# Kernel tuning notes

Measured on AMD Instinct MI355X. Metric: run time of the kernel, lower is better.

## Reference

```python
import jax, jax.numpy as jnp
import numpy as np

VOCAB, D, H = 32000, 1024, 16
DH = D // H
DFF = 4 * D
EPS = 1e-5


def layer_norm(x, g, b):
    mu = jnp.mean(x, axis=-1, keepdims=True)
    var = jnp.var(x, axis=-1, keepdims=True)
    return (x - mu) * jax.lax.rsqrt(var + EPS) * g + b


def pos_enc(seq_len, d_model):
    # faithful to the torch double-loop: angle = pos / 10000**(2*i/d) for even index i
    pos = jnp.arange(seq_len, dtype=jnp.float32)[:, None]          # [S,1]
    i_even = jnp.arange(0, d_model, 2, dtype=jnp.float32)[None, :]  # [1,D/2]
    angle = pos / jnp.power(10000.0, 2.0 * i_even / d_model)        # [S,D/2]
    pe = jnp.zeros((seq_len, d_model), dtype=jnp.float32)
    pe = pe.at[:, 0::2].set(jnp.sin(angle))
    pe = pe.at[:, 1::2].set(jnp.cos(angle))
    return pe


def setup_inputs() -> dict:
    key = jax.random.key(0)
    ks = jax.random.split(key, 16)
    s = 0.02
    return {
        "tokens": jax.random.randint(ks[0], (4, 2048), 0, VOCAB),
        "emb": jax.random.normal(ks[1], (VOCAB, D), jnp.float32) * s,
        "in_proj_w": jax.random.normal(ks[2], (3 * D, D), jnp.float32) * s,
        "in_proj_b": jnp.zeros((3 * D,), jnp.float32),
        "out_proj_w": jax.random.normal(ks[3], (D, D), jnp.float32) * s,
        "out_proj_b": jnp.zeros((D,), jnp.float32),
        "w1": jax.random.normal(ks[4], (DFF, D), jnp.float32) * s,
        "b1": jnp.zeros((DFF,), jnp.float32),
        "w2": jax.random.normal(ks[5], (D, DFF), jnp.float32) * s,
        "b2": jnp.zeros((D,), jnp.float32),
        "g1": jnp.ones((D,), jnp.float32),
        "beta1": jnp.zeros((D,), jnp.float32),
        "g2": jnp.ones((D,), jnp.float32),
        "beta2": jnp.zeros((D,), jnp.float32),
    }


def reference(tokens, emb, in_proj_w, in_proj_b, out_proj_w, out_proj_b,
              w1, b1, w2, b2, g1, beta1, g2, beta2):
    B, S = tokens.shape
    x = emb[tokens] + pos_enc(S, D)[None, :, :]                 # [B,S,D]
    # multi-head self-attention (eval mode, no dropout)
    qkv = x @ in_proj_w.T + in_proj_b                           # [B,S,3D]
    q, k, v = jnp.split(qkv, 3, axis=-1)
    q = q.reshape(B, S, H, DH)
    k = k.reshape(B, S, H, DH)
    v = v.reshape(B, S, H, DH)
    scores = jnp.einsum("bqhd,bkhd->bhqk", q, k) / jnp.sqrt(jnp.float32(DH))
    attn = jax.nn.softmax(scores, axis=-1)
    ctx = jnp.einsum("bhqk,bkhd->bqhd", attn, v).reshape(B, S, D)
    attn_out = ctx @ out_proj_w.T + out_proj_b
    h = layer_norm(x + attn_out, g1, beta1)
    ff = jax.nn.relu(h @ w1.T + b1) @ w2.T + b2
    return layer_norm(h + ff, g2, beta2)
```

## Files before the change

### kernel.cpp

```cpp
#include <hip/hip_runtime.h>
#include <math.h>

#define DMODEL 1024
#define NH 16
#define DHEAD 64
#define DFF 4096
#define BATCH 4
#define SEQ 2048
#define MROWS (BATCH * SEQ)
#define LNEPS 1e-5f
#define NT (SEQ / 64)

typedef __attribute__((ext_vector_type(8))) short bf16x8;
typedef __attribute__((ext_vector_type(4))) float f32x4;
typedef __attribute__((ext_vector_type(16))) float f32x16;
typedef __attribute__((ext_vector_type(4))) unsigned int u32x4;

__device__ inline unsigned short f2bf(float f) {
  unsigned int u = __float_as_uint(f);
  unsigned int r = (u + 0x7fffu + ((u >> 16) & 1u)) >> 16;
  return (unsigned short)r;
}

__device__ inline void gload16(const unsigned short* g, char* l) {
  __builtin_amdgcn_global_load_lds(
      (const __attribute__((address_space(1))) unsigned int*)g,
      (__attribute__((address_space(3))) unsigned int*)l, 16, 0, 0);
}

__device__ inline float fexp2(float x) {
  float r;
  asm("v_exp_f32 %0, %1" : "=v"(r) : "v"(x));
  return r;
}
__device__ inline unsigned int cvtpk(float lo, float hi) {
  unsigned int r;
  asm("v_cvt_pk_bf16_f32 %0, %1, %2" : "=v"(r) : "v"(lo), "v"(hi));
  return r;
}
__device__ inline void plswap(unsigned int& a, unsigned int& b) {
  asm("v_permlane32_swap_b32 %0, %1" : "+v"(a), "+v"(b));
}

__global__ __launch_bounds__(256)
void embed_kernel(const int* __restrict__ tokens, const float* __restrict__ emb,
                  float* __restrict__ X, unsigned short* __restrict__ Xb) {
  const int HALF = DMODEL / 2;
  int idx = blockIdx.x * 256 + threadIdx.x;
  if (idx >= MROWS * HALF) return;
  int row = idx / HALF;
  int j = idx - row * HALF;
  int s = row & (SEQ - 1);
  int tok = tokens[row];
  float2 e = ((const float2*)(emb + (size_t)tok * DMODEL))[j];
  float denom = powf(10000.0f, (2.0f * (float)(2 * j)) / (float)DMODEL);
  float ang = (float)s / denom;
  float sn, cs;
  sincosf(ang, &sn, &cs);
  float2 o;
  o.x = e.x + sn;
  o.y = e.y + cs;
  ((float2*)(X + (size_t)row * DMODEL))[j] = o;
  ushort2 ob;
  ob.x = f2bf(o.x); ob.y = f2bf(o.y);
  ((ushort2*)(Xb + (size_t)row * DMODEL))[j] = ob;
}

__global__ __launch_bounds__(256)
void cvt4_kernel(const float* __restrict__ a, const float* __restrict__ b,
                 const float* __restrict__ c, const float* __restrict__ d,
                 unsigned short* __restrict__ oa, unsigned short* __restrict__ ob,
                 unsigned short* __restrict__ oc, unsigned short* __restrict__ od) {
  int i = blockIdx.x * 256 + threadIdx.x;
  const float* src; unsigned short* dst; int off;
  if (i < 786432)       { src = a; dst = oa; off = 0; }
  else if (i < 1048576) { src = b; dst = ob; off = 786432; }
  else if (i < 2097152) { src = c; dst = oc; off = 1048576; }
  else                  { src = d; dst = od; off = 2097152; }
  int j = i - off;
  float4 v = ((const float4*)src)[j];
  ushort4 o;
  o.x = f2bf(v.x); o.y = f2bf(v.y); o.z = f2bf(v.z); o.w = f2bf(v.w);
  ((ushort4*)dst)[j] = o;
}

__device__ inline void sthalf8(const unsigned short* G, int grow0, int K, int kt,
                               char* smem_, int isB, int half, int t) {
  char* dst = smem_ + ((kt & 1) * 65536) + isB * 32768 + half * 16384;
#pragma unroll
  for (int i = 0; i < 2; ++i) {
    int g = i * 512 + t;
    int r = g >> 3, sl = g & 7;
    int c = sl ^ (r & 7);
    gload16(G + (size_t)(grow0 + half * 128 + r) * K + kt * 64 + c * 8, dst + g * 16);
  }
}

#define VM4_ asm volatile("s_waitcnt vmcnt(4)" ::: "memory")
#define VM0_ asm volatile("s_waitcnt vmcnt(0)" ::: "memory")

#define PHASE8(bufofs, MG, NP, LA, LB, STAGE_STMT, WAIT_STMT)                   \
  {                                                                             \
    if (LA) {                                                                   \
      _Pragma("unroll") for (int m = 0; m < 4; ++m) {                           \
        int arow = wm * 128 + (MG) * 64 + m * 16 + fr;                          \
        _Pragma("unroll") for (int ks = 0; ks < 2; ++ks)                        \
          af[m][ks] = *(const bf16x8*)(smem + (bufofs) + arow * 128 +           \
                        (((ks * 4 + fq) ^ (arow & 7)) * 16));                   \
      }                                                                         \
    }                                                                           \
    if (LB) {                                                                   \
      _Pragma("unroll") for (int nn = 0; nn < 2; ++nn) {                        \
        int n = (NP) * 2 + nn;                                                  \
        int brow = wn * 64 + n * 16 + fr;                                       \
        _Pragma("unroll") for (int ks = 0; ks < 2; ++ks)                        \
          bf[(NP) * 2 + nn][ks] = *(const bf16x8*)(smem + (bufofs) + 32768 +    \
                        brow * 128 + (((ks * 4 + fq) ^ (brow & 7)) * 16));      \
      }                                                                         \
    }                                                                           \
    STAGE_STMT;                                                                 \
    __builtin_amdgcn_sched_barrier(0);                                          \
    __builtin_amdgcn_s_barrier();                                               \
    asm volatile("s_waitcnt lgkmcnt(0)" ::: "memory");                          \
    __builtin_amdgcn_sched_barrier(0);                                          \
    __builtin_amdgcn_s_setprio(1);                                              \
    _Pragma("unroll") for (int m = 0; m < 4; ++m)                               \
      _Pragma("unroll") for (int nn = 0; nn < 2; ++nn)                          \
        _Pragma("unroll") for (int ks = 0; ks < 2; ++ks)                        \
          acc[(MG) * 4 + m][(NP) * 2 + nn] =                                    \
              __builtin_amdgcn_mfma_f32_16x16x32_bf16(                          \
                  af[m][ks], bf[(NP) * 2 + nn][ks],                             \
                  acc[(MG) * 4 + m][(NP) * 2 + nn], 0, 0, 0);                   \
    __builtin_amdgcn_s_setprio(0);                                              \
    WAIT_STMT;                                                                  \
    __builtin_amdgcn_sched_barrier(0);                                          \
    __builtin_amdgcn_s_barrier();                                               \
    __builtin_amdgcn_sched_barrier(0);                                          \
  }

__global__ __launch_bounds__(512, 2)
void gemm8p(const unsigned short* __restrict__ A, const unsigned short* __restrict__ B,
            const float* __restrict__ bias, const float* __restrict__ resid,
            float* __restrict__ Cf, unsigned short* __restrict__ Cb,
            int M, int N, int K, int relu) {
  extern __shared__ char smem[];

  const int t = threadIdx.x;
  const int lane = t & 63;
  const int wv = t >> 6;
  const int wm = wv >> 2;
  const int wn = wv & 3;
  const int fr = lane & 15;
  const int fq = lane >> 4;

  const int nwg = gridDim.x;
  const int orig = blockIdx.x;
  const int q8 = nwg >> 3;
  const int wgid = (orig & 7) * q8 + (orig >> 3);
  const int stid = wgid >> 2, within = wgid & 3;
  const int sm = within & 1, sn = within >> 1;
  const int Msup = M >> 9;
  const int stm = stid % Msup, stn = stid / Msup;
  const int m0 = (stm * 2 + sm) * 256;
  const int n0 = (stn * 2 + sn) * 256;

  f32x4 acc[8][4];
#pragma unroll
  for (int m = 0; m < 8; ++m)
#pragma unroll
    for (int n = 0; n < 4; ++n) acc[m][n] = (f32x4){0.f, 0.f, 0.f, 0.f};

  const int nk = K / 64;
  const int nj = nk / 2;

  sthalf8(A, m0, K, 0, smem, 0, 0, t);
  sthalf8(A, m0, K, 0, smem, 0, 1, t);
  sthalf8(B, n0, K, 0, smem, 1, 0, t);
  sthalf8(B, n0, K, 0, smem, 1, 1, t);
  sthalf8(B, n0, K, 1, smem, 1, 0, t);
  sthalf8(B, n0, K, 1, smem, 1, 1, t);
  VM4_;
  __builtin_amdgcn_sched_barrier(0);
  __builtin_amdgcn_s_barrier();
  __builtin_amdgcn_sched_barrier(0);

  bf16x8 af[4][2];
  bf16x8 bf[4][2];

  for (int j = 0; j < nj; ++j) {
    const bool st = (j + 1 < nj);
    PHASE8(0, 0, 0, 1, 1, sthalf8(A, m0, K, 2 * j + 1, smem, 0, 0, t), );
    PHASE8(0, 0, 1, 0, 1, sthalf8(A, m0, K, 2 * j + 1, smem, 0, 1, t), );
    PHASE8(0, 1, 1, 1, 0,
           if (st) sthalf8(B, n0, K, 2 * j + 2, smem, 1, 0, t), );
    PHASE8(0, 1, 0, 0, 0,
           if (st) sthalf8(B, n0, K, 2 * j + 2, smem, 1, 1, t),
           { if (st) { VM4_; } else { VM0_; } });
    PHASE8(65536, 0, 0, 1, 1,
           if (st) sthalf8(A, m0, K, 2 * j + 2, smem, 0, 0, t), );
    PHASE8(65536, 0, 1, 0, 1,
           if (st) sthalf8(A, m0, K, 2 * j + 2, smem, 0, 1, t), );
    PHASE8(65536, 1, 1, 1, 0,
           if (st) sthalf8(B, n0, K, 2 * j + 3, smem, 1, 0, t), );
    PHASE8(65536, 1, 0, 0, 0,
           if (st) sthalf8(B, n0, K, 2 * j + 3, smem, 1, 1, t),
           { if (st) { VM4_; } });
  }

  float* slab = (float*)(smem + wv * 4352);
#pragma unroll
  for (int m = 0; m < 8; ++m) {
#pragma unroll
    for (int n = 0; n < 4; ++n)
#pragma unroll
      for (int j = 0; j < 4; ++j)
        slab[(fq * 4 + j) * 68 + n * 16 + fr] = acc[m][n][j];
    int rg0 = m0 + wm * 128 + m * 16;
#pragma unroll
    for (int it = 0; it < 4; ++it) {
      int u = it * 64 + lane;
      int row = u >> 4, seg = u & 15;
      float4 v = *(const float4*)&slab[row * 68 + seg * 4];
      int col = n0 + wn * 64 + seg * 4;
      float4 b4 = *(const float4*)&bias[col];
      v.x += b4.x; v.y += b4.y; v.z += b4.z; v.w += b4.w;
      if (relu) {
        v.x = fmaxf(v.x, 0.f); v.y = fmaxf(v.y, 0.f);
        v.z = fmaxf(v.z, 0.f); v.w = fmaxf(v.w, 0.f);
      }
      size_t idx = (size_t)(rg0 + row) * N + col;
      if (resid) {
        float4 r4 = *(const float4*)&resid[idx];
        v.x += r4.x; v.y += r4.y; v.z += r4.z; v.w += r4.w;
      }
      if (Cf) {
        *(float4*)&Cf[idx] = v;
      } else {
        ushort4 ob;
        ob.x = f2bf(v.x); ob.y = f2bf(v.y); ob.z = f2bf(v.z); ob.w = f2bf(v.w);
        *(ushort4*)&Cb[idx] = ob;
      }
    }
  }
}

#define AOFF(buf) ((buf) * 49152)
#define BOFF(buf) ((buf) * 49152 + 32768)

__device__ inline void stageA(const unsigned short* Ag, char* smem_, int buf,
                              int m0, int K, int kt, int wv, int lane) {
  int rl = lane >> 3, c = (lane & 7) ^ rl;
#pragma unroll
  for (int i = 0; i < 4; ++i) {
    int r0 = (wv * 4 + i) * 8;
    gload16(Ag + (size_t)(m0 + r0 + rl) * K + kt * 64 + c * 8,
            smem_ + AOFF(buf) + r0 * 128 + lane * 16);
  }
}
__device__ inline void stageB2(const unsigned short* Bg, char* smem_, int buf,
                               int n0, int K, int kt, int wv, int lane) {
  int rl = lane >> 3, c = (lane & 7) ^ rl;
#pragma unroll
  for (int i = 0; i < 2; ++i) {
    int r0 = (wv * 2 + i) * 8;
    gload16(Bg + (size_t)(n0 + r0 + rl) * K + kt * 64 + c * 8,
            smem_ + BOFF(buf) + r0 * 128 + lane * 16);
  }
}

#define VM6 asm volatile("s_waitcnt vmcnt(6)" ::: "memory")
#define VM0 asm volatile("s_waitcnt vmcnt(0)" ::: "memory")

#define DO_PHASE(buf, mb, LOADB, STAGE_STMT, WAIT_STMT)                         \
  {                                                                             \
    bf16x8 af[2][2];                                                            \
    _Pragma("unroll") for (int mm = 0; mm < 2; ++mm) {                          \
      int arow = wm * 64 + ((mb) + mm) * 16 + fr;                               \
      _Pragma("unroll") for (int ks = 0; ks < 2; ++ks) {                        \
        int slot = (ks * 4 + fq) ^ (arow & 7);                                  \
        af[mm][ks] = *(const bf16x8*)(smem + AOFF(buf) + arow * 128 + slot * 16); \
      }                                                                         \
    }                                                                           \
    if (LOADB) {                                                                \
      _Pragma("unroll") for (int n = 0; n < 4; ++n) {                           \
        int brow = wn * 64 + n * 16 + fr;                                       \
        _Pragma("unroll") for (int ks = 0; ks < 2; ++ks) {                      \
          int slot = (ks * 4 + fq) ^ (brow & 7);                                \
          bfr[n][ks] = *(const bf16x8*)(smem + BOFF(buf) + brow * 128 + slot * 16); \
        }                                                                       \
      }                                                                         \
    }                                                                           \
    STAGE_STMT;                                                                 \
    __builtin_amdgcn_sched_barrier(0);                                          \
    __builtin_amdgcn_s_barrier();                                               \
    __builtin_amdgcn_sched_barrier(0);                                          \
    __builtin_amdgcn_s_setprio(1);                                              \
    _Pragma("unroll") for (int mm = 0; mm < 2; ++mm)                            \
      _Pragma("unroll") for (int n = 0; n < 4; ++n)                             \
        _Pragma("unroll") for (int ks = 0; ks < 2; ++ks)                        \
          acc[(mb) + mm][n] = __builtin_amdgcn_mfma_f32_16x16x32_bf16(          \
              af[mm][ks], bfr[n][ks], acc[(mb) + mm][n], 0, 0, 0);              \
    __builtin_amdgcn_s_setprio(0);                                              \
    WAIT_STMT;                                                                  \
    __builtin_amdgcn_sched_barrier(0);                                          \
    __builtin_amdgcn_s_barrier();                                               \
    __builtin_amdgcn_sched_barrier(0);                                          \
  }

__global__ __launch_bounds__(512, 2)
void gemm8(const unsigned short* __restrict__ A, const unsigned short* __restrict__ B,
           const float* __restrict__ bias, const float* __restrict__ resid,
           float* __restrict__ Cf, unsigned short* __restrict__ Cb,
           int M, int N, int K, int relu) {
  extern __shared__ char smem[];

  const int t = threadIdx.x;
  const int lane = t & 63;
  const int wv = t >> 6;
  const int wm = wv >> 1;
  const int wn = wv & 1;
  const int fr = lane & 15;
  const int fq = lane >> 4;

  const int nwg = gridDim.x;
  const int orig = blockIdx.x;
  const int q8 = nwg >> 3;
  const int wgid = (orig & 7) * q8 + (orig >> 3);
  const int stid = wgid >> 4, within = wgid & 15;
  const int sm = within & 3, sn = within >> 2;
  const int Msup = M >> 10;
  const int stm = stid % Msup, stn = stid / Msup;
  const int m0 = (stm * 4 + sm) * 256;
  const int n0 = (stn * 4 + sn) * 128;

  f32x4 acc[4][4];
#pragma unroll
  for (int m = 0; m < 4; ++m)
#pragma unroll
    for (int n = 0; n < 4; ++n) acc[m][n] = (f32x4){0.f, 0.f, 0.f, 0.f};

  const int nk = K / 64;
  const int nj = nk / 2;

  stageB2(B, smem, 0, n0, K, 0, wv, lane);
  stageA (A, smem, 0, m0, K, 0, wv, lane);
  stageB2(B, smem, 1, n0, K, 1, wv, lane);
  stageA (A, smem, 1, m0, K, 1, wv, lane);
  VM6;
  __builtin_amdgcn_sched_barrier(0);
  __builtin_amdgcn_s_barrier();
  __builtin_amdgcn_sched_barrier(0);

  for (int j = 0; j < nj - 1; ++j) {
    const int k0 = 2 * j, k1 = 2 * j + 1;
    const int s0k = k0 + 2, s1k = k1 + 2;
    const int b0 = k0 % 3, b1 = k1 % 3;
    const int sb0 = s0k % 3, sb1 = s1k % 3;
    bf16x8 bfr[4][2];
    DO_PHASE(b0, 0, true,  stageB2(B, smem, sb0, n0, K, s0k, wv, lane), );
    DO_PHASE(b0, 2, false, stageA (A, smem, sb0, m0, K, s0k, wv, lane), VM6);
    DO_PHASE(b1, 0, true,  stageB2(B, smem, sb1, n0, K, s1k, wv, lane), );
    DO_PHASE(b1, 2, false, stageA (A, smem, sb1, m0, K, s1k, wv, lane), VM6);
  }
  {
    const int b0 = (nk - 2) % 3, b1 = (nk - 1) % 3;
    bf16x8 bfr[4][2];
    DO_PHASE(b0, 0, true,  , );
    DO_PHASE(b0, 2, false, , VM0);
    DO_PHASE(b1, 0, true,  , );
    DO_PHASE(b1, 2, false, , );
  }

  float* slab = (float*)(smem + wv * 4352);
#pragma unroll
  for (int m = 0; m < 4; ++m) {
#pragma unroll
    for (int n = 0; n < 4; ++n)
#pragma unroll
      for (int j = 0; j < 4; ++j)
        slab[(fq * 4 + j) * 68 + n * 16 + fr] = acc[m][n][j];
    int rg0 = m0 + wm * 64 + m * 16;
#pragma unroll
    for (int it = 0; it < 4; ++it) {
      int u = it * 64 + lane;
      int row = u >> 4, seg = u & 15;
      float4 v = *(const float4*)&slab[row * 68 + seg * 4];
      int col = n0 + wn * 64 + seg * 4;
      float4 b4 = *(const float4*)&bias[col];
      v.x += b4.x; v.y += b4.y; v.z += b4.z; v.w += b4.w;
      if (relu) {
        v.x = fmaxf(v.x, 0.f); v.y = fmaxf(v.y, 0.f);
        v.z = fmaxf(v.z, 0.f); v.w = fmaxf(v.w, 0.f);
      }
      size_t idx = (size_t)(rg0 + row) * N + col;
      if (resid) {
        float4 r4 = *(const float4*)&resid[idx];
        v.x += r4.x; v.y += r4.y; v.z += r4.z; v.w += r4.w;
      }
      if (Cf) {
        *(float4*)&Cf[idx] = v;
      } else {
        ushort4 ob;
        ob.x = f2bf(v.x); ob.y = f2bf(v.y); ob.z = f2bf(v.z); ob.w = f2bf(v.w);
        *(ushort4*)&Cb[idx] = ob;
      }
    }
  }
}

__global__ __launch_bounds__(256)
void vtrans_kernel(const unsigned short* __restrict__ qkvb, unsigned short* __restrict__ vtb) {
  __shared__ __align__(16) unsigned short tile[64][64];
  const int st = blockIdx.x;
  const int bh = blockIdx.y;
  const int b = bh >> 4, h = bh & 15;
  const int t = threadIdx.x;
#pragma unroll
  for (int p = 0; p < 2; ++p) {
    int item = p * 256 + t;
    int r = item >> 3, c8 = item & 7;
    const unsigned short* src =
        qkvb + (size_t)(b * SEQ + st * 64 + r) * (3 * DMODEL) + 2048 + h * 64 + c8 * 8;
    *(uint4*)&tile[r][(c8 ^ (r & 7)) * 8] = *(const uint4*)src;
  }
  __syncthreads();
#pragma unroll
  for (int p = 0; p < 2; ++p) {
    int item = p * 256 + t;
    int d = item & 63, s8 = item >> 6;
    unsigned short v[8];
#pragma unroll
    for (int e = 0; e < 8; ++e) {
      int s = s8 * 8 + e;
      v[e] = tile[s][(((d >> 3) ^ (s & 7)) * 8) + (d & 7)];
    }
    uint4 u;
    u.x = (unsigned int)v[0] | ((unsigned int)v[1] << 16);
    u.y = (unsigned int)v[2] | ((unsigned int)v[3] << 16);
    u.z = (unsigned int)v[4] | ((unsigned int)v[5] << 16);
    u.w = (unsigned int)v[6] | ((unsigned int)v[7] << 16);
    *(uint4*)(vtb + ((size_t)bh * 64 + d) * SEQ + st * 64 + s8 * 8) = u;
  }
}

__global__ __launch_bounds__(512, 4)
void attn_kernel(const unsigned short* __restrict__ qkv, const unsigned short* __restrict__ vtb,
                 unsigned short* __restrict__ ctxb) {
  __shared__ __align__(16) unsigned short Ks[2][64][64];
  __shared__ __align__(16) unsigned short Vts[2][64][64];
  __shared__ __align__(16) unsigned short Slab[8][32][64];

  const int t = threadIdx.x;
  const int lane = t & 63;
  const int wq = t >> 6;
  const int l31 = lane & 31;
  const int hi1 = lane >> 5;
  const int bid = blockIdx.x;
  const int bh = bid & 63;
  const int qt = bid >> 6;
  const int b = bh >> 4, h = bh & 15;
  const int q0 = qt * 256;

  const size_t RS = 3 * DMODEL;
  const unsigned short* qb = qkv + (size_t)b * SEQ * RS + h * DHEAD;
  const unsigned short* kb = qb + DMODEL;

  bf16x8 qf[4];
  {
    const unsigned short* qrow = qb + (size_t)(q0 + wq * 32 + l31) * RS;
#pragma unroll
    for (int s = 0; s < 4; ++s)
      qf[s] = *(const bf16x8*)(qrow + s * 16 + hi1 * 8);
  }

  const unsigned short* kgl =
      kb + (size_t)(wq * 8 + (lane >> 3)) * RS + ((lane & 7) ^ (lane >> 3)) * 8;
  const unsigned short* vgl =
      vtb + ((size_t)bh * 64 + wq * 8 + (lane >> 3)) * SEQ + ((lane & 7) ^ (lane >> 3)) * 8;

  f32x16 oacc[2] = {};
  float lacc = 0.f;

  gload16(kgl, (char*)&Ks[0][wq * 8][0]);
  gload16(vgl, (char*)&Vts[0][wq * 8][0]);
  __syncthreads();

  const float C = 0.18033688011112042f;

  for (int kt = 0; kt < NT; ++kt) {
    const int cur = kt & 1;
    if (kt + 1 < NT) {
      gload16(kgl + (size_t)(kt + 1) * 64 * RS, (char*)&Ks[cur ^ 1][wq * 8][0]);
      gload16(vgl + (size_t)(kt + 1) * 64, (char*)&Vts[cur ^ 1][wq * 8][0]);
    }

    f32x16 sacc[2] = {};
    __builtin_amdgcn_s_setprio(1);
#pragma unroll
    for (int s = 0; s < 4; ++s) {
#pragma unroll
      for (int kvt = 0; kvt < 2; ++kvt) {
        int row = kvt * 32 + l31;
        bf16x8 kf = *(const bf16x8*)&Ks[cur][row][(((2 * s + hi1) ^ (row & 7)) * 8)];
        sacc[kvt] = __builtin_amdgcn_mfma_f32_32x32x16_bf16(kf, qf[s], sacc[kvt], 0, 0, 0);
      }
    }
    __builtin_amdgcn_s_setprio(0);

#pragma unroll
    for (int kvt = 0; kvt < 2; ++kvt) {
      float p[16];
#pragma unroll
      for (int r = 0; r < 16; ++r) p[r] = fexp2(sacc[kvt][r] * C);
      float ps = 0.f;
#pragma unroll
      for (int r = 0; r < 16; ++r) ps += p[r];
      lacc += ps;
#pragma unroll
      for (int half = 0; half < 2; ++half) {
        const int lo = half * 8;
        unsigned int x0 = cvtpk(p[lo + 0], p[lo + 1]);
        unsigned int x1 = cvtpk(p[lo + 2], p[lo + 3]);
        unsigned int y0 = cvtpk(p[lo + 4], p[lo + 5]);
        unsigned int y1 = cvtpk(p[lo + 6], p[lo + 7]);
        plswap(x0, y0);
        plswap(x1, y1);
        bf16x8 pa = __builtin_bit_cast(bf16x8, (u32x4){x0, x1, y0, y1});
        const int s2 = kvt * 2 + half;
        __builtin_amdgcn_s_setprio(1);
#pragma unroll
        for (int dt = 0; dt < 2; ++dt) {
          int vrow = dt * 32 + l31;
          bf16x8 vf = *(const bf16x8*)&Vts[cur][vrow][(((2 * s2 + hi1) ^ (vrow & 7)) * 8)];
          oacc[dt] = __builtin_amdgcn_mfma_f32_32x32x16_bf16(pa, vf, oacc[dt], 0, 0, 0);
        }
        __builtin_amdgcn_s_setprio(0);
      }
    }
    __syncthreads();
  }

  lacc += __shfl_xor(lacc, 32);
  float inv = 1.0f / lacc;

  float iv[16];
#pragma unroll
  for (int r = 0; r < 16; ++r)
    iv[r] = __shfl(inv, (r & 3) + 8 * (r >> 2) + 4 * hi1);

#pragma unroll
  for (int dt = 0; dt < 2; ++dt) {
    const int chunk = dt * 4 + (l31 >> 3);
    const int e7 = l31 & 7;
#pragma unroll
    for (int r = 0; r < 16; ++r) {
      int qp = (r & 3) + 8 * (r >> 2) + 4 * hi1;
      Slab[wq][qp][((chunk ^ (qp & 7)) * 8) + e7] = f2bf(oacc[dt][r] * iv[r]);
    }
  }
#pragma unroll
  for (int it = 0; it < 4; ++it) {
    int u = it * 64 + lane;
    int row = u >> 3, s = u & 7;
    uint4 v = *(const uint4*)&Slab[wq][row][((s ^ (row & 7)) * 8)];
    *(uint4*)(ctxb + (size_t)(b * SEQ + q0 + wq * 32 + row) * DMODEL + h * DHEAD + s * 8) = v;
  }
}

__global__ __launch_bounds__(256)
void ln_kernel(const float* __restrict__ Z, const float* __restrict__ g,
               const float* __restrict__ bta, float* __restrict__ Y,
               unsigned short* __restrict__ Yb) {
  const int row = blockIdx.x;
  const float4* z4 = (const float4*)(Z + (size_t)row * DMODEL);
  float4 v = z4[threadIdx.x];
  float s = v.x + v.y + v.z + v.w;
  float ss = fmaf(v.x, v.x, fmaf(v.y, v.y, fmaf(v.z, v.z, v.w * v.w)));
#pragma unroll
  for (int o = 32; o >= 1; o >>= 1) {
    s += __shfl_xor(s, o);
    ss += __shfl_xor(ss, o);
  }
  __shared__ float red[8];
  int w = threadIdx.x >> 6;
  if ((threadIdx.x & 63) == 0) { red[w] = s; red[4 + w] = ss; }
  __syncthreads();
  s = red[0] + red[1] + red[2] + red[3];
  ss = red[4] + red[5] + red[6] + red[7];
  float mu = s * (1.0f / DMODEL);
  float var = ss * (1.0f / DMODEL) - mu * mu;
  float rs = rsqrtf(var + LNEPS);
  float4 gg = ((const float4*)g)[threadIdx.x];
  float4 bb = ((const float4*)bta)[threadIdx.x];
  float4 o;
  o.x = (v.x - mu) * rs * gg.x + bb.x;
  o.y = (v.y - mu) * rs * gg.y + bb.y;
  o.z = (v.z - mu) * rs * gg.z + bb.z;
  o.w = (v.w - mu) * rs * gg.w + bb.w;
  ((float4*)(Y + (size_t)row * DMODEL))[threadIdx.x] = o;
  if (Yb) {
    ushort4 ob;
    ob.x = f2bf(o.x); ob.y = f2bf(o.y); ob.z = f2bf(o.z); ob.w = f2bf(o.w);
    ((ushort4*)(Yb + (size_t)row * DMODEL))[threadIdx.x] = ob;
  }
}

extern "C" void kernel_launch(void* const* d_in, const int* in_sizes, int n_in,
                              void* d_out, int out_size, void* d_ws, size_t ws_size,
                              hipStream_t stream) {
  const int* tokens       = (const int*)d_in[0];
  const float* emb        = (const float*)d_in[1];
  const float* in_proj_w  = (const float*)d_in[2];
  const float* in_proj_b  = (const float*)d_in[3];
  const float* out_proj_w = (const float*)d_in[4];
  const float* out_proj_b = (const float*)d_in[5];
  const float* w1         = (const float*)d_in[6];
  const float* b1         = (const float*)d_in[7];
  const float* w2         = (const float*)d_in[8];
  const float* b2         = (const float*)d_in[9];
  const float* g1         = (const float*)d_in[10];
  const float* beta1      = (const float*)d_in[11];
  const float* g2         = (const float*)d_in[12];
  const float* beta2      = (const float*)d_in[13];
  float* out = (float*)d_out;

  char* ws = (char*)d_ws;
  const size_t MB = 1ull << 20;
  unsigned short* inwb  = (unsigned short*)(ws + 0 * MB);
  unsigned short* outwb = (unsigned short*)(ws + 6 * MB);
  unsigned short* w1b   = (unsigned short*)(ws + 8 * MB);
  unsigned short* w2b   = (unsigned short*)(ws + 16 * MB);
  float* x              = (float*)(ws + 24 * MB);
  unsigned short* xb    = (unsigned short*)(ws + 56 * MB);
  unsigned short* qkvb  = (unsigned short*)(ws + 72 * MB);
  unsigned short* vtb   = (unsigned short*)(ws + 120 * MB);
  unsigned short* ctxb  = (unsigned short*)(ws + 56 * MB);
  float* h              = (float*)(ws + 72 * MB);
  unsigned short* hb    = (unsigned short*)(ws + 104 * MB);
  unsigned short* ffbb  = (unsigned short*)(ws + 120 * MB);
  float* y2             = (float*)(ws + 24 * MB);

  const size_t GLDS8 = 147456;
  const size_t GLDSP = 131072;

  embed_kernel<<<(MROWS * (DMODEL / 2) + 255) / 256, 256, 0, stream>>>(tokens, emb, x, xb);
  cvt4_kernel<<<12288, 256, 0, stream>>>(in_proj_w, out_proj_w, w1, w2,
                                         inwb, outwb, w1b, w2b);
  gemm8p<<<(MROWS / 256) * (3 * DMODEL / 256), 512, GLDSP, stream>>>(
      xb, inwb, in_proj_b, nullptr, nullptr, qkvb, MROWS, 3 * DMODEL, DMODEL, 0);
  vtrans_kernel<<<dim3(SEQ / 64, BATCH * NH), 256, 0, stream>>>(qkvb, vtb);
  attn_kernel<<<(SEQ / 256) * (BATCH * NH), 512, 0, stream>>>(qkvb, vtb, ctxb);
  gemm8<<<(MROWS / 256) * (DMODEL / 128), 512, GLDS8, stream>>>(
      ctxb, outwb, out_proj_b, x, h, nullptr, MROWS, DMODEL, DMODEL, 0);
  ln_kernel<<<MROWS, 256, 0, stream>>>(h, g1, beta1, h, hb);
  gemm8p<<<(MROWS / 256) * (DFF / 256), 512, GLDSP, stream>>>(
      hb, w1b, b1, nullptr, nullptr, ffbb, MROWS, DFF, DMODEL, 1);
  gemm8<<<(MROWS / 256) * (DMODEL / 128), 512, GLDS8, stream>>>(
      ffbb, w2b, b2, h, y2, nullptr, MROWS, DMODEL, DFF, 0);
  ln_kernel<<<MROWS, 256, 0, stream>>>(y2, g2, beta2, out, nullptr);
}
```

Measured before the change: 400.9 us.

## Process two query subtiles per warp in attention to reuse K/V fragments

Each attention workgroup now covers 512 query rows instead of 256, with every warp holding two 32-row query fragments and two sets of accumulators. Each K and V fragment read from LDS feeds two MFMAs, halving the K/V global loads and LDS reads per query. The grid shrinks to 256 blocks. Register pressure doubles, so launch bounds drop to 2 blocks per CU, which reduces occupancy and the ability to hide latency.

Result: no change. 407.7 us (+1.7%).

```diff
diff --git a/kernel.cpp b/kernel.cpp
--- a/kernel.cpp
+++ b/kernel.cpp
@@ -443,7 +443,7 @@
   }
 }
 
-__global__ __launch_bounds__(512, 4)
+__global__ __launch_bounds__(512, 2)
 void attn_kernel(const unsigned short* __restrict__ qkv, const unsigned short* __restrict__ vtb,
                  unsigned short* __restrict__ ctxb) {
   __shared__ __align__(16) unsigned short Ks[2][64][64];
@@ -459,18 +459,21 @@
   const int bh = bid & 63;
   const int qt = bid >> 6;
   const int b = bh >> 4, h = bh & 15;
-  const int q0 = qt * 256;
+  const int q0 = qt * 512;
 
   const size_t RS = 3 * DMODEL;
   const unsigned short* qb = qkv + (size_t)b * SEQ * RS + h * DHEAD;
   const unsigned short* kb = qb + DMODEL;
 
-  bf16x8 qf[4];
+  bf16x8 qf0[4], qf1[4];
   {
-    const unsigned short* qrow = qb + (size_t)(q0 + wq * 32 + l31) * RS;
-#pragma unroll
-    for (int s = 0; s < 4; ++s)
-      qf[s] = *(const bf16x8*)(qrow + s * 16 + hi1 * 8);
+    const unsigned short* qr0 = qb + (size_t)(q0 + wq * 64 + l31) * RS;
+    const unsigned short* qr1 = qr0 + 32 * RS;
+#pragma unroll
+    for (int s = 0; s < 4; ++s) {
+      qf0[s] = *(const bf16x8*)(qr0 + s * 16 + hi1 * 8);
+      qf1[s] = *(const bf16x8*)(qr1 + s * 16 + hi1 * 8);
+    }
   }
 
   const unsigned short* kgl =
@@ -478,8 +481,9 @@
   const unsigned short* vgl =
       vtb + ((size_t)bh * 64 + wq * 8 + (lane >> 3)) * SEQ + ((lane & 7) ^ (lane >> 3)) * 8;
 
-  f32x16 oacc[2] = {};
-  float lacc = 0.f;
+  f32x16 oacc0[2] = {};
+  f32x16 oacc1[2] = {};
+  float lacc0 = 0.f, lacc1 = 0.f;
 
   gload16(kgl, (char*)&Ks[0][wq * 8][0]);
   gload16(vgl, (char*)&Vts[0][wq * 8][0]);
@@ -494,7 +498,8 @@
       gload16(vgl + (size_t)(kt + 1) * 64, (char*)&Vts[cur ^ 1][wq * 8][0]);
     }
 
-    f32x16 sacc[2] = {};
+    f32x16 sacc0[2] = {};
+    f32x16 sacc1[2] = {};
     __builtin_amdgcn_s_setprio(1);
 #pragma unroll
     for (int s = 0; s < 4; ++s) {
@@ -502,68 +507,98 @@
       for (int kvt = 0; kvt < 2; ++kvt) {
         int row = kvt * 32 + l31;
         bf16x8 kf = *(const bf16x8*)&Ks[cur][row][(((2 * s + hi1) ^ (row & 7)) * 8)];
-        sacc[kvt] = __builtin_amdgcn_mfma_f32_32x32x16_bf16(kf, qf[s], sacc[kvt], 0, 0, 0);
+        sacc0[kvt] = __builtin_amdgcn_mfma_f32_32x32x16_bf16(kf, qf0[s], sacc0[kvt], 0, 0, 0);
+        sacc1[kvt] = __builtin_amdgcn_mfma_f32_32x32x16_bf16(kf, qf1[s], sacc1[kvt], 0, 0, 0);
       }
     }
     __builtin_amdgcn_s_setprio(0);
 
+    bf16x8 pa0[4], pa1[4];
 #pragma unroll
     for (int kvt = 0; kvt < 2; ++kvt) {
-      float p[16];
-#pragma unroll
-      for (int r = 0; r < 16; ++r) p[r] = fexp2(sacc[kvt][r] * C);
-      float ps = 0.f;
-#pragma unroll
-      for (int r = 0; r < 16; ++r) ps += p[r];
-      lacc += ps;
+      float p0[16], p1[16];
+#pragma unroll
+      for (int r = 0; r < 16; ++r) p0[r] = fexp2(sacc0[kvt][r] * C);
+#pragma unroll
+      for (int r = 0; r < 16; ++r) p1[r] = fexp2(sacc1[kvt][r] * C);
+      float ps0 = 0.f, ps1 = 0.f;
+#pragma unroll
+      for (int r = 0; r < 16; ++r) { ps0 += p0[r]; ps1 += p1[r]; }
+      lacc0 += ps0;
+      lacc1 += ps1;
 #pragma unroll
       for (int half = 0; half < 2; ++half) {
         const int lo = half * 8;
-        unsigned int x0 = cvtpk(p[lo + 0], p[lo + 1]);
-        unsigned int x1 = cvtpk(p[lo + 2], p[lo + 3]);
-        unsigned int y0 = cvtpk(p[lo + 4], p[lo + 5]);
-        unsigned int y1 = cvtpk(p[lo + 6], p[lo + 7]);
-        plswap(x0, y0);
-        plswap(x1, y1);
-        bf16x8 pa = __builtin_bit_cast(bf16x8, (u32x4){x0, x1, y0, y1});
-        const int s2 = kvt * 2 + half;
-        __builtin_amdgcn_s_setprio(1);
-#pragma unroll
-        for (int dt = 0; dt < 2; ++dt) {
-          int vrow = dt * 32 + l31;
-          bf16x8 vf = *(const bf16x8*)&Vts[cur][vrow][(((2 * s2 + hi1) ^ (vrow & 7)) * 8)];
-          oacc[dt] = __builtin_amdgcn_mfma_f32_32x32x16_bf16(pa, vf, oacc[dt], 0, 0, 0);
+        {
+          unsigned int x0 = cvtpk(p0[lo + 0], p0[lo + 1]);
+          unsigned int x1 = cvtpk(p0[lo + 2], p0[lo + 3]);
+          unsigned int y0 = cvtpk(p0[lo + 4], p0[lo + 5]);
+          unsigned int y1 = cvtpk(p0[lo + 6], p0[lo + 7]);
+          plswap(x0, y0);
+          plswap(x1, y1);
+          pa0[kvt * 2 + half] = __builtin_bit_cast(bf16x8, (u32x4){x0, x1, y0, y1});
         }
-        __builtin_amdgcn_s_setprio(0);
-      }
-    }
+        {
+          unsigned int x0 = cvtpk(p1[lo + 0], p1[lo + 1]);
+          unsigned int x1 = cvtpk(p1[lo + 2], p1[lo + 3]);
+          unsigned int y0 = cvtpk(p1[lo + 4], p1[lo + 5]);
+          unsigned int y1 = cvtpk(p1[lo + 6], p1[lo + 7]);
+          plswap(x0, y0);
+          plswap(x1, y1);
+          pa1[kvt * 2 + half] = __builtin_bit_cast(bf16x8, (u32x4){x0, x1, y0, y1});
+        }
+      }
+    }
+
+    __builtin_amdgcn_s_setprio(1);
+#pragma unroll
+    for (int s2 = 0; s2 < 4; ++s2) {
+#pragma unroll
+      for (int dt = 0; dt < 2; ++dt) {
+        int vrow = dt * 32 + l31;
+        bf16x8 vf = *(const bf16x8*)&Vts[cur][vrow][(((2 * s2 + hi1) ^ (vrow & 7)) * 8)];
+        oacc0[dt] = __builtin_amdgcn_mfma_f32_32x32x16_bf16(pa0[s2], vf, oacc0[dt], 0, 0, 0);
+        oacc1[dt] = __builtin_amdgcn_mfma_f32_32x32x16_bf16(pa1[s2], vf, oacc1[dt], 0, 0, 0);
+      }
+    }
+    __builtin_amdgcn_s_setprio(0);
     __syncthreads();
   }
 
-  lacc += __shfl_xor(lacc, 32);
-  float inv = 1.0f / lacc;
-
-  float iv[16];
-#pragma unroll
-  for (int r = 0; r < 16; ++r)
-    iv[r] = __shfl(inv, (r & 3) + 8 * (r >> 2) + 4 * hi1);
-
-#pragma unroll
-  for (int dt = 0; dt < 2; ++dt) {
-    const int chunk = dt * 4 + (l31 >> 3);
-    const int e7 = l31 & 7;
-#pragma unroll
-    for (int r = 0; r < 16; ++r) {
-      int qp = (r & 3) + 8 * (r >> 2) + 4 * hi1;
-      Slab[wq][qp][((chunk ^ (qp & 7)) * 8) + e7] = f2bf(oacc[dt][r] * iv[r]);
-    }
-  }
-#pragma unroll
-  for (int it = 0; it < 4; ++it) {
-    int u = it * 64 + lane;
-    int row = u >> 3, s = u & 7;
-    uint4 v = *(const uint4*)&Slab[wq][row][((s ^ (row & 7)) * 8)];
-    *(uint4*)(ctxb + (size_t)(b * SEQ + q0 + wq * 32 + row) * DMODEL + h * DHEAD + s * 8) = v;
+  lacc0 += __shfl_xor(lacc0, 32);
+  lacc1 += __shfl_xor(lacc1, 32);
+  float inv0 = 1.0f / lacc0;
+  float inv1 = 1.0f / lacc1;
+
+  float iv0[16], iv1[16];
+#pragma unroll
+  for (int r = 0; r < 16; ++r) {
+    int qp = (r & 3) + 8 * (r >> 2) + 4 * hi1;
+    iv0[r] = __shfl(inv0, qp);
+    iv1[r] = __shfl(inv1, qp);
+  }
+
+#pragma unroll
+  for (int qi = 0; qi < 2; ++qi) {
+#pragma unroll
+    for (int dt = 0; dt < 2; ++dt) {
+      const int chunk = dt * 4 + (l31 >> 3);
+      const int e7 = l31 & 7;
+#pragma unroll
+      for (int r = 0; r < 16; ++r) {
+        int qp = (r & 3) + 8 * (r >> 2) + 4 * hi1;
+        float val = (qi == 0) ? oacc0[dt][r] * iv0[r] : oacc1[dt][r] * iv1[r];
+        Slab[wq][qp][((chunk ^ (qp & 7)) * 8) + e7] = f2bf(val);
+      }
+    }
+#pragma unroll
+    for (int it = 0; it < 4; ++it) {
+      int u = it * 64 + lane;
+      int row = u >> 3, s = u & 7;
+      uint4 v = *(const uint4*)&Slab[wq][row][((s ^ (row & 7)) * 8)];
+      *(uint4*)(ctxb + (size_t)(b * SEQ + q0 + wq * 64 + qi * 32 + row) * DMODEL +
+                h * DHEAD + s * 8) = v;
+    }
   }
 }
 
@@ -649,7 +684,7 @@
   gemm8p<<<(MROWS / 256) * (3 * DMODEL / 256), 512, GLDSP, stream>>>(
       xb, inwb, in_proj_b, nullptr, nullptr, qkvb, MROWS, 3 * DMODEL, DMODEL, 0);
   vtrans_kernel<<<dim3(SEQ / 64, BATCH * NH), 256, 0, stream>>>(qkvb, vtb);
-  attn_kernel<<<(SEQ / 256) * (BATCH * NH), 512, 0, stream>>>(qkvb, vtb, ctxb);
+  attn_kernel<<<(SEQ / 512) * (BATCH * NH), 512, 0, stream>>>(qkvb, vtb, ctxb);
   gemm8<<<(MROWS / 256) * (DMODEL / 128), 512, GLDS8, stream>>>(
       ctxb, outwb, out_proj_b, x, h, nullptr, MROWS, DMODEL, DMODEL, 0);
   ln_kernel<<<MROWS, 256, 0, stream>>>(h, g1, beta1, h, hb);
```

## Rewrite N=1024 GEMM with 8-phase double-buffered pipeline and smaller LDS

Applied to the files above, without the earlier changes.

Replaces the triple-buffered 4-phase gemm8 used for the out-projection and FFN2 GEMMs with a gemm8p128 kernel. It mirrors the 8-phase ping-pong schedule of gemm8p, using two LDS buffers (96KB instead of 144KB) and staging A and B in half-tile chunks interleaved across eight MFMA phases. It also changes the workgroup swizzle from 4x4 to 2x2 supertiles and adds an explicit lgkmcnt wait after each barrier. The aim is finer overlap of global loads with MFMA and lower LDS use, at the cost of less prefetch depth and more barriers.

Measured after the change: 401.1 us. No clear change (+0.0%).

```diff
diff --git a/kernel.cpp b/kernel.cpp
--- a/kernel.cpp
+++ b/kernel.cpp
@@ -97,6 +97,7 @@
 }
 
 #define VM4_ asm volatile("s_waitcnt vmcnt(4)" ::: "memory")
+#define VM2_ asm volatile("s_waitcnt vmcnt(2)" ::: "memory")
 #define VM0_ asm volatile("s_waitcnt vmcnt(0)" ::: "memory")
 
 #define PHASE8(bufofs, MG, NP, LA, LB, STAGE_STMT, WAIT_STMT)                   \
@@ -244,62 +245,61 @@
   }
 }
 
-#define AOFF(buf) ((buf) * 49152)
-#define BOFF(buf) ((buf) * 49152 + 32768)
-
-__device__ inline void stageA(const unsigned short* Ag, char* smem_, int buf,
-                              int m0, int K, int kt, int wv, int lane) {
-  int rl = lane >> 3, c = (lane & 7) ^ rl;
-#pragma unroll
-  for (int i = 0; i < 4; ++i) {
-    int r0 = (wv * 4 + i) * 8;
-    gload16(Ag + (size_t)(m0 + r0 + rl) * K + kt * 64 + c * 8,
-            smem_ + AOFF(buf) + r0 * 128 + lane * 16);
-  }
-}
-__device__ inline void stageB2(const unsigned short* Bg, char* smem_, int buf,
-                               int n0, int K, int kt, int wv, int lane) {
-  int rl = lane >> 3, c = (lane & 7) ^ rl;
+__device__ inline void stA128(const unsigned short* G, int m0, int K, int kt,
+                              int half, char* smem_, int t) {
+  char* dst = smem_ + ((kt & 1) * 49152) + half * 16384;
 #pragma unroll
   for (int i = 0; i < 2; ++i) {
-    int r0 = (wv * 2 + i) * 8;
-    gload16(Bg + (size_t)(n0 + r0 + rl) * K + kt * 64 + c * 8,
-            smem_ + BOFF(buf) + r0 * 128 + lane * 16);
-  }
-}
-
-#define VM6 asm volatile("s_waitcnt vmcnt(6)" ::: "memory")
-#define VM0 asm volatile("s_waitcnt vmcnt(0)" ::: "memory")
-
-#define DO_PHASE(buf, mb, LOADB, STAGE_STMT, WAIT_STMT)                         \
+    int g = i * 512 + t;
+    int r = g >> 3, sl = g & 7;
+    int c = sl ^ (r & 7);
+    gload16(G + (size_t)(m0 + half * 128 + r) * K + kt * 64 + c * 8, dst + g * 16);
+  }
+}
+__device__ inline void stB128(const unsigned short* G, int n0, int K, int kt,
+                              char* smem_, int t) {
+  char* dst = smem_ + ((kt & 1) * 49152) + 32768;
+#pragma unroll
+  for (int i = 0; i < 2; ++i) {
+    int g = i * 512 + t;
+    int r = g >> 3, sl = g & 7;
+    int c = sl ^ (r & 7);
+    gload16(G + (size_t)(n0 + r) * K + kt * 64 + c * 8, dst + g * 16);
+  }
+}
+
+#define PH128(bufofs, MG, NP, LA, LB, STAGE_STMT, WAIT_STMT)                    \
   {                                                                             \
-    bf16x8 af[2][2];                                                            \
-    _Pragma("unroll") for (int mm = 0; mm < 2; ++mm) {                          \
-      int arow = wm * 64 + ((mb) + mm) * 16 + fr;                               \
-      _Pragma("unroll") for (int ks = 0; ks < 2; ++ks) {                        \
-        int slot = (ks * 4 + fq) ^ (arow & 7);                                  \
-        af[mm][ks] = *(const bf16x8*)(smem + AOFF(buf) + arow * 128 + slot * 16); \
+    if (LA) {                                                                   \
+      _Pragma("unroll") for (int mm = 0; mm < 2; ++mm) {                        \
+        int arow = wm * 64 + ((MG) * 2 + mm) * 16 + fr;                         \
+        _Pragma("unroll") for (int ks = 0; ks < 2; ++ks)                        \
+          af[mm][ks] = *(const bf16x8*)(smem + (bufofs) + arow * 128 +          \
+                        (((ks * 4 + fq) ^ (arow & 7)) * 16));                   \
       }                                                                         \
     }                                                                           \
-    if (LOADB) {                                                                \
-      _Pragma("unroll") for (int n = 0; n < 4; ++n) {                           \
+    if (LB) {                                                                   \
+      _Pragma("unroll") for (int nn = 0; nn < 2; ++nn) {                        \
+        int n = (NP) * 2 + nn;                                                  \
         int brow = wn * 64 + n * 16 + fr;                                       \
-        _Pragma("unroll") for (int ks = 0; ks < 2; ++ks) {                      \
-          int slot = (ks * 4 + fq) ^ (brow & 7);                                \
-          bfr[n][ks] = *(const bf16x8*)(smem + BOFF(buf) + brow * 128 + slot * 16); \
-        }                                                                       \
+        _Pragma("unroll") for (int ks = 0; ks < 2; ++ks)                        \
+          bf[(NP) * 2 + nn][ks] = *(const bf16x8*)(smem + (bufofs) + 32768 +    \
+                        brow * 128 + (((ks * 4 + fq) ^ (brow & 7)) * 16));      \
       }                                                                         \
     }                                                                           \
     STAGE_STMT;                                                                 \
     __builtin_amdgcn_sched_barrier(0);                                          \
     __builtin_amdgcn_s_barrier();                                               \
+    asm volatile("s_waitcnt lgkmcnt(0)" ::: "memory");                          \
     __builtin_amdgcn_sched_barrier(0);                                          \
     __builtin_amdgcn_s_setprio(1);                                              \
     _Pragma("unroll") for (int mm = 0; mm < 2; ++mm)                            \
-      _Pragma("unroll") for (int n = 0; n < 4; ++n)                             \
+      _Pragma("unroll") for (int nn = 0; nn < 2; ++nn)                          \
         _Pragma("unroll") for (int ks = 0; ks < 2; ++ks)                        \
-          acc[(mb) + mm][n] = __builtin_amdgcn_mfma_f32_16x16x32_bf16(          \
-              af[mm][ks], bfr[n][ks], acc[(mb) + mm][n], 0, 0, 0);              \
+          acc[(MG) * 2 + mm][(NP) * 2 + nn] =                                   \
+              __builtin_amdgcn_mfma_f32_16x16x32_bf16(                          \
+                  af[mm][ks], bf[(NP) * 2 + nn][ks],                            \
+                  acc[(MG) * 2 + mm][(NP) * 2 + nn], 0, 0, 0);                  \
     __builtin_amdgcn_s_setprio(0);                                              \
     WAIT_STMT;                                                                  \
     __builtin_amdgcn_sched_barrier(0);                                          \
@@ -308,10 +308,10 @@
   }
 
 __global__ __launch_bounds__(512, 2)
-void gemm8(const unsigned short* __restrict__ A, const unsigned short* __restrict__ B,
-           const float* __restrict__ bias, const float* __restrict__ resid,
-           float* __restrict__ Cf, unsigned short* __restrict__ Cb,
-           int M, int N, int K, int relu) {
+void gemm8p128(const unsigned short* __restrict__ A, const unsigned short* __restrict__ B,
+               const float* __restrict__ bias, const float* __restrict__ resid,
+               float* __restrict__ Cf, unsigned short* __restrict__ Cb,
+               int M, int N, int K, int relu) {
   extern __shared__ char smem[];
 
   const int t = threadIdx.x;
@@ -326,12 +326,12 @@
   const int orig = blockIdx.x;
   const int q8 = nwg >> 3;
   const int wgid = (orig & 7) * q8 + (orig >> 3);
-  const int stid = wgid >> 4, within = wgid & 15;
-  const int sm = within & 3, sn = within >> 2;
-  const int Msup = M >> 10;
+  const int stid = wgid >> 2, within = wgid & 3;
+  const int sm = within & 1, sn = within >> 1;
+  const int Msup = M >> 9;
   const int stm = stid % Msup, stn = stid / Msup;
-  const int m0 = (stm * 4 + sm) * 256;
-  const int n0 = (stn * 4 + sn) * 128;
+  const int m0 = (stm * 2 + sm) * 256;
+  const int n0 = (stn * 2 + sn) * 128;
 
   f32x4 acc[4][4];
 #pragma unroll
@@ -342,33 +342,35 @@
   const int nk = K / 64;
   const int nj = nk / 2;
 
-  stageB2(B, smem, 0, n0, K, 0, wv, lane);
-  stageA (A, smem, 0, m0, K, 0, wv, lane);
-  stageB2(B, smem, 1, n0, K, 1, wv, lane);
-  stageA (A, smem, 1, m0, K, 1, wv, lane);
-  VM6;
+  stA128(A, m0, K, 0, 0, smem, t);
+  stA128(A, m0, K, 0, 1, smem, t);
+  stB128(B, n0, K, 0, smem, t);
+  stB128(B, n0, K, 1, smem, t);
+  VM2_;
   __builtin_amdgcn_sched_barrier(0);
   __builtin_amdgcn_s_barrier();
   __builtin_amdgcn_sched_barrier(0);
 
-  for (int j = 0; j < nj - 1; ++j) {
-    const int k0 = 2 * j, k1 = 2 * j + 1;
-    const int s0k = k0 + 2, s1k = k1 + 2;
-    const int b0 = k0 % 3, b1 = k1 % 3;
-    const int sb0 = s0k % 3, sb1 = s1k % 3;
-    bf16x8 bfr[4][2];
-    DO_PHASE(b0, 0, true,  stageB2(B, smem, sb0, n0, K, s0k, wv, lane), );
-    DO_PHASE(b0, 2, false, stageA (A, smem, sb0, m0, K, s0k, wv, lane), VM6);
-    DO_PHASE(b1, 0, true,  stageB2(B, smem, sb1, n0, K, s1k, wv, lane), );
-    DO_PHASE(b1, 2, false, stageA (A, smem, sb1, m0, K, s1k, wv, lane), VM6);
-  }
-  {
-    const int b0 = (nk - 2) % 3, b1 = (nk - 1) % 3;
-    bf16x8 bfr[4][2];
-    DO_PHASE(b0, 0, true,  , );
-    DO_PHASE(b0, 2, false, , VM0);
-    DO_PHASE(b1, 0, true,  , );
-    DO_PHASE(b1, 2, false, , );
+  bf16x8 af[2][2];
+  bf16x8 bf[4][2];
+
+  for (int j = 0; j < nj; ++j) {
+    const bool st = (j + 1 < nj);
+    const int k1 = 2 * j + 1;
+    PH128(0, 0, 0, 1, 1, stA128(A, m0, K, k1, 0, smem, t), );
+    PH128(0, 0, 1, 0, 1, stA128(A, m0, K, k1, 1, smem, t), );
+    PH128(0, 1, 0, 1, 0,
+          if (st) stB128(B, n0, K, k1 + 1, smem, t), );
+    PH128(0, 1, 1, 0, 0,
+          if (st) stA128(A, m0, K, k1 + 1, 0, smem, t),
+          { if (st) { VM4_; } else { VM0_; } });
+    PH128(49152, 0, 0, 1, 1,
+          if (st) stA128(A, m0, K, k1 + 1, 1, smem, t), );
+    PH128(49152, 0, 1, 0, 1, , );
+    PH128(49152, 1, 0, 1, 0,
+          if (st) stB128(B, n0, K, k1 + 2, smem, t), );
+    PH128(49152, 1, 1, 0, 0, ,
+          { if (st) { VM2_; } });
   }
 
   float* slab = (float*)(smem + wv * 4352);
@@ -640,8 +642,8 @@
   unsigned short* ffbb  = (unsigned short*)(ws + 120 * MB);
   float* y2             = (float*)(ws + 24 * MB);
 
-  const size_t GLDS8 = 147456;
-  const size_t GLDSP = 131072;
+  const size_t GLDSP  = 131072;
+  const size_t GLDSPN = 98304;
 
   embed_kernel<<<(MROWS * (DMODEL / 2) + 255) / 256, 256, 0, stream>>>(tokens, emb, x, xb);
   cvt4_kernel<<<12288, 256, 0, stream>>>(in_proj_w, out_proj_w, w1, w2,
@@ -650,12 +652,12 @@
       xb, inwb, in_proj_b, nullptr, nullptr, qkvb, MROWS, 3 * DMODEL, DMODEL, 0);
   vtrans_kernel<<<dim3(SEQ / 64, BATCH * NH), 256, 0, stream>>>(qkvb, vtb);
   attn_kernel<<<(SEQ / 256) * (BATCH * NH), 512, 0, stream>>>(qkvb, vtb, ctxb);
-  gemm8<<<(MROWS / 256) * (DMODEL / 128), 512, GLDS8, stream>>>(
+  gemm8p128<<<(MROWS / 256) * (DMODEL / 128), 512, GLDSPN, stream>>>(
       ctxb, outwb, out_proj_b, x, h, nullptr, MROWS, DMODEL, DMODEL, 0);
   ln_kernel<<<MROWS, 256, 0, stream>>>(h, g1, beta1, h, hb);
   gemm8p<<<(MROWS / 256) * (DFF / 256), 512, GLDSP, stream>>>(
       hb, w1b, b1, nullptr, nullptr, ffbb, MROWS, DFF, DMODEL, 1);
-  gemm8<<<(MROWS / 256) * (DMODEL / 128), 512, GLDS8, stream>>>(
+  gemm8p128<<<(MROWS / 256) * (DMODEL / 128), 512, GLDSPN, stream>>>(
       ffbb, w2b, b2, h, y2, nullptr, MROWS, DMODEL, DFF, 0);
   ln_kernel<<<MROWS, 256, 0, stream>>>(y2, g2, beta2, out, nullptr);
 }
```
